# Performance work log

Hardware: AMD Instinct MI355X
Metric: run time of the kernel (lower is better)

Reference implementation:

```python
import jax, jax.numpy as jnp
import numpy as np

B, T, I, R, O = 1, 2048, 8, 4096, 8
SPECTRAL_RADIUS = 0.9
SPARSITY = 0.1


def setup_inputs() -> dict:
    key = jax.random.key(0)
    k1, k2, k3, k4, k5, k6 = jax.random.split(key, 6)
    x = jax.random.normal(k1, (B, T, I), dtype=jnp.float32)
    Win = jax.random.normal(k2, (R, I), dtype=jnp.float32)
    W = jax.random.normal(k3, (R, R), dtype=jnp.float32)
    # sparse mask + spectral-radius scaling (circular-law approx: rho(sparse gaussian) ~ sqrt(sparsity*R))
    mask = (jax.random.uniform(k4, (R, R)) < SPARSITY).astype(jnp.float32)
    W = W * mask * (SPECTRAL_RADIUS / jnp.sqrt(SPARSITY * R))
    Wout_w = jax.random.normal(k5, (O, R), dtype=jnp.float32) / jnp.sqrt(R)
    Wout_b = jax.random.normal(k6, (O,), dtype=jnp.float32) * 0.01
    return {"x": x, "Win": Win, "W": W, "Wout_w": Wout_w, "Wout_b": Wout_b}


def reference(x, Win, W, Wout_w, Wout_b):
    Bb = x.shape[0]
    h0 = jnp.zeros((Bb, W.shape[0]), dtype=x.dtype)

    def step(h, xt):  # xt: [B, I]
        h = jnp.tanh(xt @ Win.T + h @ W.T)          # [B, R]
        out = h @ Wout_w.T + Wout_b                  # [B, O]
        return h, out

    xs = jnp.swapaxes(x, 0, 1)                       # [T, B, I]
    _, outs = jax.lax.scan(step, h0, xs)             # outs: [T, B, O]
    return jnp.swapaxes(outs, 0, 1)                  # [B, T, O]
```

## Files before the change

kernel.cpp:

```cpp
#include <hip/hip_runtime.h>
#include <math.h>


#define T_STEPS 2048
#define R_DIM   4096
#define I_DIM   8
#define O_DIM   8
#define NWG     64
#define ROWS_PER_WG (R_DIM / NWG)
#define HALF_ROWS 32
#define POOL_CAP 16384
#define BLOCK    1024
#define NS       36

typedef float v4f __attribute__((ext_vector_type(4)));

__device__ float        g_hist[(size_t)T_STEPS * R_DIM];
__device__ unsigned int g_flag[NWG * 32];

__global__ void esn_init_kernel() {
    for (int i = threadIdx.x; i < NWG * 32; i += blockDim.x)
        __hip_atomic_store(&g_flag[i], 0u, __ATOMIC_RELAXED,
                           __HIP_MEMORY_SCOPE_SYSTEM);
}

__launch_bounds__(BLOCK, 1)
__global__ void esn_recur_kernel(const float* __restrict__ x,
                                 const float* __restrict__ Win,
                                 const float* __restrict__ W) {
    __shared__ uint2 s_pool[POOL_CAP];
    __shared__ float s_h[R_DIM];
    __shared__ int   s_start[HALF_ROWS + 1];
    __shared__ int   s_cnt[HALF_ROWS];
    __shared__ float s_win[ROWS_PER_WG][I_DIM];

    const int wg   = blockIdx.x;
    const int tid  = threadIdx.x;
    const int lane = tid & 63;
    const int wave = tid >> 6;
    const int row0 = wg * ROWS_PER_WG;

    const int row16 = tid >> 4;
    const int sub   = tid & 15;

    float    rv[NS];
    unsigned ri[NS / 2];

    for (int pass = 0; pass < 2; ++pass) {
        const int prow0 = row0 + pass * HALF_ROWS;
        for (int rr = wave; rr < HALF_ROWS; rr += 16) {
            const float* wrow = W + (size_t)(prow0 + rr) * R_DIM;
            int cnt = 0;
            for (int base = 0; base < R_DIM; base += 64) {
                float v = wrow[base + lane];
                cnt += __popcll(__ballot(v != 0.0f));
            }
            if (lane == 0) s_cnt[rr] = cnt;
        }
        __syncthreads();
        if (tid == 0) {
            int acc = 0;
            for (int rr = 0; rr < HALF_ROWS; ++rr) {
                s_start[rr] = (acc < POOL_CAP) ? acc : POOL_CAP;
                acc += s_cnt[rr];
            }
            s_start[HALF_ROWS] = (acc < POOL_CAP) ? acc : POOL_CAP;
        }
        __syncthreads();
        for (int rr = wave; rr < HALF_ROWS; rr += 16) {
            const float* wrow = W + (size_t)(prow0 + rr) * R_DIM;
            int off = s_start[rr];
            for (int base = 0; base < R_DIM; base += 64) {
                float v = wrow[base + lane];
                unsigned long long m = __ballot(v != 0.0f);
                int pre = __popcll(m & ((1ull << lane) - 1ull));
                if (v != 0.0f) {
                    int pos = off + pre;
                    if (pos < POOL_CAP) {
                        s_pool[pos].x = __float_as_uint(v);
                        s_pool[pos].y = (base + lane) * 4;
                    }
                }
                off += __popcll(m);
            }
        }
        __syncthreads();
        const int lr = row16 - pass * HALF_ROWS;
        if (lr >= 0 && lr < HALF_ROWS) {
            const int st = s_start[lr];
            const int en = s_start[lr + 1];
            #pragma unroll
            for (int m = 0; m < NS; ++m) {
                const int e = st + sub + (m << 4);
                float    v = 0.0f;
                unsigned b = 0u;
                if (e < en) { uint2 p = s_pool[e]; v = __uint_as_float(p.x); b = p.y; }
                rv[m] = v;
                if ((m & 1) == 0) ri[m >> 1] = b;
                else              ri[m >> 1] |= (b << 16);
            }
        }
        __syncthreads();
    }
    if (tid < ROWS_PER_WG * I_DIM) {
        int rr = tid / I_DIM, c = tid % I_DIM;
        s_win[rr][c] = Win[(size_t)(row0 + rr) * I_DIM + c];
    }
    __syncthreads();

    const int  src_wg  = (wave << 2) + (lane & 3);
    const bool poller  = (lane < 4);
    const unsigned* fp = &g_flag[src_wg << 5];

    for (int t = 0; t < T_STEPS; ++t) {
        const float4* xp = (const float4*)(x + (size_t)t * I_DIM);
        const float4 xa = xp[0];
        const float4 xb = xp[1];

        if (t > 0) {
            const unsigned ut = (unsigned)t;
            for (;;) {
                unsigned v = poller
                    ? __hip_atomic_load(fp, __ATOMIC_RELAXED,
                                        __HIP_MEMORY_SCOPE_SYSTEM)
                    : ut;
                if (__all(v >= ut)) break;
                __builtin_amdgcn_s_sleep(1);
            }
            const v4f* bp = (const v4f*)(g_hist + (size_t)(t - 1) * R_DIM
                                         + (size_t)tid * 4);
            v4f r0;
            asm volatile(
                "global_load_dwordx4 %0, %1, off sc0 sc1\n\t"
                "s_waitcnt vmcnt(0)"
                : "=v"(r0)
                : "v"(bp)
                : "memory");
            *(v4f*)(s_h + (size_t)tid * 4) = r0;
            __syncthreads();
        }

        float acc = 0.0f;
        if (t > 0) {
            #pragma unroll
            for (int m = 0; m < NS; ++m) {
                const unsigned ba = (m & 1) ? (ri[m >> 1] >> 16)
                                            : (ri[m >> 1] & 0xffffu);
                const float hv = *(const float*)((const char*)s_h + ba);
                acc += rv[m] * hv;
            }
        }
        acc += __shfl_xor(acc, 8, 16);
        acc += __shfl_xor(acc, 4, 16);
        acc += __shfl_xor(acc, 2, 16);
        acc += __shfl_xor(acc, 1, 16);

        if (sub == 0) {
            float a = acc;
            a += s_win[row16][0] * xa.x;
            a += s_win[row16][1] * xa.y;
            a += s_win[row16][2] * xa.z;
            a += s_win[row16][3] * xa.w;
            a += s_win[row16][4] * xb.x;
            a += s_win[row16][5] * xb.y;
            a += s_win[row16][6] * xb.z;
            a += s_win[row16][7] * xb.w;
            float h = tanhf(a);
            __hip_atomic_store(&g_hist[(size_t)t * R_DIM + row0 + row16], h,
                               __ATOMIC_RELAXED, __HIP_MEMORY_SCOPE_SYSTEM);
        }
        asm volatile("s_waitcnt vmcnt(0)" ::: "memory");
        __syncthreads();
        if (tid == 0)
            __hip_atomic_store(&g_flag[wg << 5], (unsigned)(t + 1),
                               __ATOMIC_RELAXED, __HIP_MEMORY_SCOPE_SYSTEM);
    }
}

__global__ void esn_out_kernel(const float* __restrict__ Wout_w,
                               const float* __restrict__ Wout_b,
                               float* __restrict__ out) {
    const int t = blockIdx.x;
    const int lane = threadIdx.x;
    const float* hp = g_hist + (size_t)t * R_DIM;
    float acc[O_DIM];
    #pragma unroll
    for (int o = 0; o < O_DIM; ++o) acc[o] = 0.0f;
    for (int i = lane; i < R_DIM; i += 256) {
        float h0 = __hip_atomic_load(hp + i,       __ATOMIC_RELAXED, __HIP_MEMORY_SCOPE_SYSTEM);
        float h1 = __hip_atomic_load(hp + i + 64,  __ATOMIC_RELAXED, __HIP_MEMORY_SCOPE_SYSTEM);
        float h2 = __hip_atomic_load(hp + i + 128, __ATOMIC_RELAXED, __HIP_MEMORY_SCOPE_SYSTEM);
        float h3 = __hip_atomic_load(hp + i + 192, __ATOMIC_RELAXED, __HIP_MEMORY_SCOPE_SYSTEM);
        #pragma unroll
        for (int o = 0; o < O_DIM; ++o) acc[o] += h0 * Wout_w[(size_t)o * R_DIM + i];
        #pragma unroll
        for (int o = 0; o < O_DIM; ++o) acc[o] += h1 * Wout_w[(size_t)o * R_DIM + i + 64];
        #pragma unroll
        for (int o = 0; o < O_DIM; ++o) acc[o] += h2 * Wout_w[(size_t)o * R_DIM + i + 128];
        #pragma unroll
        for (int o = 0; o < O_DIM; ++o) acc[o] += h3 * Wout_w[(size_t)o * R_DIM + i + 192];
    }
    #pragma unroll
    for (int o = 0; o < O_DIM; ++o) {
        float a = acc[o];
        a += __shfl_xor(a, 32);
        a += __shfl_xor(a, 16);
        a += __shfl_xor(a, 8);
        a += __shfl_xor(a, 4);
        a += __shfl_xor(a, 2);
        a += __shfl_xor(a, 1);
        if (lane == 0) out[(size_t)t * O_DIM + o] = a + Wout_b[o];
    }
}

extern "C" void kernel_launch(void* const* d_in, const int* in_sizes, int n_in,
                              void* d_out, int out_size, void* d_ws, size_t ws_size,
                              hipStream_t stream) {
    const float* x    = (const float*)d_in[0];
    const float* Win  = (const float*)d_in[1];
    const float* W    = (const float*)d_in[2];
    const float* Ww   = (const float*)d_in[3];
    const float* Wb   = (const float*)d_in[4];
    float* out = (float*)d_out;

    hipLaunchKernelGGL(esn_init_kernel, dim3(1), dim3(256), 0, stream);

    void* args[] = { (void*)&x, (void*)&Win, (void*)&W };
    hipLaunchCooperativeKernel((void*)esn_recur_kernel, dim3(NWG), dim3(BLOCK),
                               args, 0, stream);

    hipLaunchKernelGGL(esn_out_kernel, dim3(T_STEPS), dim3(64), 0, stream,
                       Ww, Wb, out);
}
```

Before: 7.061 ms.

## Replace per-step barrier flag with per-wave arrival counters and fused poll-load

Each wave now bumps its workgroup's flag with an atomic add once its stores have drained, so the block-wide barrier before publishing is no longer needed. Consumers wait for a count of 16 per step instead of the step index. Each thread polls only the flag of the workgroup whose hidden-state slice it reads, and issues that flag read together with the data load in one round trip. This removes a barrier and a serialized flag-then-data memory latency from every recurrence step. The cost is more atomic traffic, and there is an ordering risk: the data load is issued before the flag load, so stale data could in principle be accepted.

```diff
diff --git a/kernel.cpp b/kernel.cpp
--- a/kernel.cpp
+++ b/kernel.cpp
@@ -108,9 +108,7 @@
     }
     __syncthreads();
 
-    const int  src_wg  = (wave << 2) + (lane & 3);
-    const bool poller  = (lane < 4);
-    const unsigned* fp = &g_flag[src_wg << 5];
+    const unsigned* fsrc = &g_flag[(tid >> 4) << 5];
 
     for (int t = 0; t < T_STEPS; ++t) {
         const float4* xp = (const float4*)(x + (size_t)t * I_DIM);
@@ -118,24 +116,21 @@
         const float4 xb = xp[1];
 
         if (t > 0) {
-            const unsigned ut = (unsigned)t;
+            const unsigned need = (unsigned)t << 4;
+            const float* hp = g_hist + (size_t)(t - 1) * R_DIM
+                              + (size_t)tid * 4;
+            v4f r0; unsigned fv;
             for (;;) {
-                unsigned v = poller
-                    ? __hip_atomic_load(fp, __ATOMIC_RELAXED,
-                                        __HIP_MEMORY_SCOPE_SYSTEM)
-                    : ut;
-                if (__all(v >= ut)) break;
-                __builtin_amdgcn_s_sleep(1);
-            }
-            const v4f* bp = (const v4f*)(g_hist + (size_t)(t - 1) * R_DIM
-                                         + (size_t)tid * 4);
-            v4f r0;
-            asm volatile(
-                "global_load_dwordx4 %0, %1, off sc0 sc1\n\t"
-                "s_waitcnt vmcnt(0)"
-                : "=v"(r0)
-                : "v"(bp)
-                : "memory");
+                asm volatile(
+                    "global_load_dwordx4 %0, %2, off sc0 sc1\n\t"
+                    "global_load_dword %1, %3, off sc0 sc1\n\t"
+                    "s_waitcnt vmcnt(0)"
+                    : "=v"(r0), "=v"(fv)
+                    : "v"(hp), "v"(fsrc)
+                    : "memory");
+                if (__all(fv >= need)) break;
+                __builtin_amdgcn_s_sleep(2);
+            }
             *(v4f*)(s_h + (size_t)tid * 4) = r0;
             __syncthreads();
         }
@@ -170,10 +165,11 @@
                                __ATOMIC_RELAXED, __HIP_MEMORY_SCOPE_SYSTEM);
         }
         asm volatile("s_waitcnt vmcnt(0)" ::: "memory");
-        __syncthreads();
-        if (tid == 0)
-            __hip_atomic_store(&g_flag[wg << 5], (unsigned)(t + 1),
-                               __ATOMIC_RELAXED, __HIP_MEMORY_SCOPE_SYSTEM);
+        if (lane == 0)
+            (void)__hip_atomic_fetch_add(&g_flag[wg << 5], 1u,
+                                         __ATOMIC_RELAXED,
+                                         __HIP_MEMORY_SCOPE_SYSTEM);
+        __syncthreads();
     }
 }
 
```

After: 8.340 ms. +18.1%, slower.
